# Kernel optimization log

Measured on AMD Instinct MI355X. Metric: run time of the kernel, lower is better.

The kernel has to match this reference:

```python
import jax, jax.numpy as jnp
import numpy as np

COMMITMENT_COST = 0.25
NUM_EMBEDDINGS = 1024
EMBEDDING_DIM = 256


def setup_inputs() -> dict:
    key = jax.random.key(0)
    k1, k2 = jax.random.split(key)
    inputs = jax.random.normal(k1, (64, 256, 32, 32), dtype=jnp.float32)
    emb_w = jax.random.normal(k2, (NUM_EMBEDDINGS, EMBEDDING_DIM), dtype=jnp.float32)
    return {"inputs": inputs, "emb_w": emb_w}


def reference(inputs, emb_w):
    # NCHW -> NHWC, flatten to [N, D]
    x = jnp.transpose(inputs, (0, 2, 3, 1))  # [B, H, W, D]
    B, H, W, D = x.shape
    flat = x.reshape(-1, D)  # [N, D]

    distances = (
        jnp.sum(flat * flat, axis=1, keepdims=True)
        + jnp.sum(emb_w * emb_w, axis=1)
        - 2.0 * flat @ emb_w.T
    )
    idx = jnp.argmin(distances, axis=1)  # [N]

    # one-hot @ W is just a gather of codebook rows
    quantized = emb_w[idx].reshape(B, H, W, D)

    # avg_probs = mean of one-hot encodings = normalized codeword counts
    counts = jnp.zeros((NUM_EMBEDDINGS,), dtype=jnp.float32).at[idx].add(1.0)
    avg_probs = counts / flat.shape[0]
    perplexity = jnp.exp(-jnp.sum(avg_probs * jnp.log(avg_probs + 1e-10)))

    e_latent_loss = jnp.mean((jax.lax.stop_gradient(quantized) - x) ** 2)
    loss = COMMITMENT_COST * e_latent_loss

    # straight-through estimator
    quantized_st = x + jax.lax.stop_gradient(quantized - x)
    quantized_out = jnp.transpose(quantized_st, (0, 3, 1, 2))  # back to NCHW

    return loss, quantized_out, perplexity, idx.reshape(B, H, W)
```

## Files before the change

### kernel.cpp

```cpp
#include <hip/hip_runtime.h>
#include <hip/hip_bf16.h>
#include <math.h>

typedef _Float16 f16;
typedef __attribute__((ext_vector_type(8))) _Float16 f16x8;
typedef __attribute__((ext_vector_type(16))) float f32x16;

#define DIMS 256
#define NCODE 1024
#define NPTS 65536

#define OUT_Q_OFF 1
#define OUT_PERP_OFF 16777217
#define OUT_IDX_OFF 16777218

#define EHI_F32_OFF 4
#define ELO_F32_OFF (4 + 131072)
#define TILE_BYTES 16384

#define XSTRIDE 132

__device__ __forceinline__ void gload_lds16(const void* g, void* l) {
    __builtin_amdgcn_global_load_lds(
        (const __attribute__((address_space(1))) unsigned int*)g,
        (__attribute__((address_space(3))) unsigned int*)l, 16, 0, 0);
}

__global__ __launch_bounds__(256) void k_eprep(const float* __restrict__ ew,
                                               char* __restrict__ ehi,
                                               char* __restrict__ elo,
                                               float* __restrict__ enorm) {
    int w = threadIdx.x >> 6;
    int l = threadIdx.x & 63;
    int row = blockIdx.x * 4 + w;
    float4 v = *reinterpret_cast<const float4*>(ew + (size_t)row * DIMS + l * 4);
    float vv[4] = {v.x, v.y, v.z, v.w};
    __align__(8) f16 hh[4];
    __align__(8) f16 ll[4];
    float s = 0.0f;
    #pragma unroll
    for (int e = 0; e < 4; ++e) {
        f16 h = (f16)vv[e];
        hh[e] = h;
        ll[e] = (f16)(vv[e] - (float)h);
        s += vv[e] * vv[e];
    }
    size_t off = (size_t)(row >> 5) * TILE_BYTES + (size_t)(row & 31) * 512
               + (size_t)((((l >> 1) ^ (row & 7)) << 4) + ((l & 1) << 3));
    *reinterpret_cast<float2*>(ehi + off) = *reinterpret_cast<float2*>(hh);
    *reinterpret_cast<float2*>(elo + off) = *reinterpret_cast<float2*>(ll);
    #pragma unroll
    for (int off2 = 32; off2 > 0; off2 >>= 1) s += __shfl_down(s, off2);
    if (l == 0) enorm[row] = s;
}

__global__ __launch_bounds__(256, 2) void k_argmin_mfma(const float* __restrict__ x,
                                                        const char* __restrict__ ehi,
                                                        const char* __restrict__ elo,
                                                        const float* __restrict__ enorm,
                                                        int* __restrict__ out_idx) {
    __shared__ __align__(16) char smem[2 * 2 * TILE_BYTES];
    __shared__ float enorm_lds[NCODE];
    float* Xs = (float*)smem;

    const int t = threadIdx.x;
    const int wave = t >> 6;
    const int lane = t & 63;
    const int lrow = lane & 31;
    const int lhalf = lane >> 5;

    const int blk = blockIdx.x;
    const int b = blk >> 3;
    const int hw0 = (blk & 7) << 7;
    const float* xb = x + (size_t)b * (DIMS * 1024) + hw0;

    #pragma unroll
    for (int i = 0; i < 4; ++i) enorm_lds[t + 256 * i] = enorm[t + 256 * i];

    f16x8 ahi[16], alo[16];
    #pragma unroll
    for (int dc = 0; dc < 4; ++dc) {
        __syncthreads();
        #pragma unroll
        for (int i = 0; i < 8; ++i) {
            int d = (t >> 5) + 8 * i;
            int p4 = (t & 31) * 4;
            float4 v = *reinterpret_cast<const float4*>(xb + (size_t)(dc * 64 + d) * 1024 + p4);
            *reinterpret_cast<float4*>(&Xs[d * XSTRIDE + p4]) = v;
        }
        __syncthreads();
        int p = wave * 32 + lrow;
        #pragma unroll
        for (int kcl = 0; kcl < 4; ++kcl) {
            f16x8 h, l;
            #pragma unroll
            for (int e = 0; e < 8; ++e) {
                float xv = Xs[(kcl * 16 + lhalf * 8 + e) * XSTRIDE + p];
                f16 hi = (f16)xv;
                h[e] = hi;
                l[e] = (f16)(xv - (float)hi);
            }
            ahi[dc * 4 + kcl] = h;
            alo[dc * 4 + kcl] = l;
        }
    }
    __syncthreads();

    const char* gplane = (wave >> 1) ? elo : ehi;
    const int pl_off = (wave >> 1) * TILE_BYTES;
    const int woff = (wave & 1) * 8192;

    #pragma unroll
    for (int i = 0; i < 8; ++i) {
        int off = woff + i * 1024;
        gload_lds16(gplane + off + lane * 16, smem + pl_off + off);
    }
    __syncthreads();

    float bestv[16];
    int besti[16];
    #pragma unroll
    for (int r = 0; r < 16; ++r) { bestv[r] = 3.4e38f; besti[r] = 0; }

#define ROUND_BODY(ACC_CUR, ACC_PREV, RD)                                         \
    {                                                                             \
        const int rd_ = (RD);                                                     \
        const int cur_ = rd_ & 1;                                                 \
        if (rd_ + 1 < 32) {                                                       \
            const char* gp_ = gplane + (size_t)(rd_ + 1) * TILE_BYTES;            \
            char* lp_ = smem + (cur_ ^ 1) * (2 * TILE_BYTES) + pl_off;            \
            _Pragma("unroll")                                                     \
            for (int i_ = 0; i_ < 8; ++i_) {                                      \
                int off_ = woff + i_ * 1024;                                      \
                gload_lds16(gp_ + off_ + lane * 16, lp_ + off_);                  \
            }                                                                     \
        }                                                                         \
        const char* EHb_ = smem + cur_ * (2 * TILE_BYTES);                        \
        const char* ELb_ = EHb_ + TILE_BYTES;                                     \
        _Pragma("unroll")                                                         \
        for (int r_ = 0; r_ < 16; ++r_) ACC_CUR[r_] = 0.0f;                       \
        __builtin_amdgcn_s_setprio(1);                                            \
        _Pragma("unroll")                                                         \
        for (int kc_ = 0; kc_ < 16; ++kc_) {                                      \
            int g_ = kc_ * 2 + lhalf;                                             \
            int ra_ = lrow * 512 + ((g_ ^ (lrow & 7)) << 4);                      \
            f16x8 bh_ = *reinterpret_cast<const f16x8*>(EHb_ + ra_);              \
            f16x8 bl_ = *reinterpret_cast<const f16x8*>(ELb_ + ra_);              \
            ACC_CUR = __builtin_amdgcn_mfma_f32_32x32x16_f16(ahi[kc_], bh_, ACC_CUR, 0, 0, 0); \
            ACC_CUR = __builtin_amdgcn_mfma_f32_32x32x16_f16(ahi[kc_], bl_, ACC_CUR, 0, 0, 0); \
            ACC_CUR = __builtin_amdgcn_mfma_f32_32x32x16_f16(alo[kc_], bh_, ACC_CUR, 0, 0, 0); \
        }                                                                         \
        __builtin_amdgcn_s_setprio(0);                                            \
        if (rd_ > 0) {                                                            \
            const int pc0_ = (rd_ - 1) * 32;                                      \
            float en_ = enorm_lds[pc0_ + lrow];                                   \
            int cw_ = pc0_ + lrow;                                                \
            _Pragma("unroll")                                                     \
            for (int r_ = 0; r_ < 16; ++r_) {                                     \
                float s_ = fmaf(-2.0f, ACC_PREV[r_], en_);                        \
                if (s_ < bestv[r_]) { bestv[r_] = s_; besti[r_] = cw_; }          \
            }                                                                     \
        }                                                                         \
        __syncthreads();                                                          \
    }

    f32x16 accA, accB;
    for (int rr = 0; rr < 16; ++rr) {
        ROUND_BODY(accA, accB, 2 * rr);
        ROUND_BODY(accB, accA, 2 * rr + 1);
    }
    {
        float en = enorm_lds[31 * 32 + lrow];
        int cw = 31 * 32 + lrow;
        #pragma unroll
        for (int r = 0; r < 16; ++r) {
            float s = fmaf(-2.0f, accB[r], en);
            if (s < bestv[r]) { bestv[r] = s; besti[r] = cw; }
        }
    }
#undef ROUND_BODY

    #pragma unroll
    for (int off = 1; off <= 16; off <<= 1) {
        #pragma unroll
        for (int r = 0; r < 16; ++r) {
            float ov = __shfl_xor(bestv[r], off);
            int oi = __shfl_xor(besti[r], off);
            if (ov < bestv[r] || (ov == bestv[r] && oi < besti[r])) {
                bestv[r] = ov;
                besti[r] = oi;
            }
        }
    }
    if (lrow == 0) {
        #pragma unroll
        for (int r = 0; r < 16; ++r) {
            int row = (r & 3) + 8 * (r >> 2) + 4 * lhalf;
            out_idx[blk * 128 + wave * 32 + row] = besti[r];
        }
    }
}

#define QSTRIDE 258
__global__ __launch_bounds__(512) void k_quant(const float* __restrict__ x,
                                               const float* __restrict__ ew,
                                               const int* __restrict__ idxv,
                                               float* __restrict__ out,
                                               float* __restrict__ loss_acc,
                                               int* __restrict__ counts) {
    __shared__ float Eq[64 * QSTRIDE];
    __shared__ int ids[64];
    __shared__ int h[NCODE];
    const int t = threadIdx.x;
    const int blk = blockIdx.x;
    const int b = blk >> 4;
    const int hw0 = (blk & 15) << 6;

    if (t < 64) ids[t] = idxv[(b << 10) + hw0 + t];
    h[t] = 0;
    h[t + 512] = 0;
    __syncthreads();

    if (t < 64) atomicAdd(&h[ids[t]], 1);

    #pragma unroll
    for (int i = 0; i < 8; ++i) {
        int f = i * 512 + t;
        int row = f >> 6;
        int c4 = f & 63;
        float4 v = *reinterpret_cast<const float4*>(ew + (size_t)ids[row] * DIMS + c4 * 4);
        float2 lo2 = {v.x, v.y};
        float2 hi2 = {v.z, v.w};
        *reinterpret_cast<float2*>(&Eq[row * QSTRIDE + c4 * 4]) = lo2;
        *reinterpret_cast<float2*>(&Eq[row * QSTRIDE + c4 * 4 + 2]) = hi2;
    }
    __syncthreads();

    const int q4 = t & 15;
    const int cb = t >> 4;
    const int p = q4 * 4;
    float lsum = 0.0f;
    #pragma unroll
    for (int k = 0; k < 8; ++k) {
        int c = k * 32 + cb;
        unsigned g = ((unsigned)b << 18) | ((unsigned)c << 10) | (unsigned)(hw0 + p);
        float4 xv = *reinterpret_cast<const float4*>(x + g);
        float q0 = Eq[(p + 0) * QSTRIDE + c];
        float q1 = Eq[(p + 1) * QSTRIDE + c];
        float q2 = Eq[(p + 2) * QSTRIDE + c];
        float q3 = Eq[(p + 3) * QSTRIDE + c];
        float d0 = q0 - xv.x, d1 = q1 - xv.y, d2 = q2 - xv.z, d3 = q3 - xv.w;
        out[OUT_Q_OFF + g + 0] = xv.x + d0;
        out[OUT_Q_OFF + g + 1] = xv.y + d1;
        out[OUT_Q_OFF + g + 2] = xv.z + d2;
        out[OUT_Q_OFF + g + 3] = xv.w + d3;
        lsum += d0 * d0 + d1 * d1 + d2 * d2 + d3 * d3;
    }
    #pragma unroll
    for (int off = 32; off > 0; off >>= 1) lsum += __shfl_down(lsum, off);
    if ((t & 63) == 0) atomicAdd(&loss_acc[blk & 63], lsum);

    int v0 = h[t];
    if (v0) atomicAdd(&counts[t], v0);
    int v1 = h[t + 512];
    if (v1) atomicAdd(&counts[t + 512], v1);
    if (t < 64) out[OUT_IDX_OFF + (b << 10) + hw0 + t] = (float)ids[t];
}

__global__ __launch_bounds__(256) void k_final(const int* __restrict__ counts,
                                               const float* __restrict__ loss_acc,
                                               float* __restrict__ out) {
    int t = threadIdx.x;
    float s = 0.0f;
    #pragma unroll
    for (int i = 0; i < 4; ++i) {
        int cnt = counts[t + 256 * i];
        float p = (float)cnt * (1.0f / 65536.0f);
        s += p * logf(p + 1e-10f);
    }
    #pragma unroll
    for (int off = 32; off > 0; off >>= 1) s += __shfl_down(s, off);
    __shared__ float wsum[4];
    if ((t & 63) == 0) wsum[t >> 6] = s;
    __syncthreads();
    if (t == 0) {
        float S = wsum[0] + wsum[1] + wsum[2] + wsum[3];
        out[OUT_PERP_OFF] = expf(-S);
        float ls = 0.0f;
        for (int i = 0; i < 64; ++i) ls += loss_acc[i];
        out[0] = 0.25f * (ls * (1.0f / 16777216.0f));
    }
}

extern "C" void kernel_launch(void* const* d_in, const int* in_sizes, int n_in,
                              void* d_out, int out_size, void* d_ws, size_t ws_size,
                              hipStream_t stream) {
    const float* x = (const float*)d_in[0];
    const float* ew = (const float*)d_in[1];
    float* out = (float*)d_out;
    float* ws = (float*)d_ws;

    float* loss_acc = ws;
    int* counts = (int*)(ws + 64);
    float* enorm = ws + 64 + 1024;
    int* idxv = (int*)(ws + 64 + 2048);

    char* ehi = (char*)(out + EHI_F32_OFF);
    char* elo = (char*)(out + ELO_F32_OFF);

    hipMemsetAsync(d_ws, 0, (64 + 1024) * sizeof(float), stream);

    k_eprep<<<256, 256, 0, stream>>>(ew, ehi, elo, enorm);
    k_argmin_mfma<<<512, 256, 0, stream>>>(x, ehi, elo, enorm, idxv);
    k_quant<<<1024, 512, 0, stream>>>(x, ew, idxv, out, loss_acc, counts);
    k_final<<<1, 256, 0, stream>>>(counts, loss_acc, out);
}
```

Measured before the change: 173.4 us.

## Fold codebook norm into MFMA init, fuse final reduction, rework quant access

The argmin kernel now seeds each accumulator with -0.5*||e||^2 and tracks a maximum, so the per-element fma in the compare loop goes away. The separate single-block finalize kernel is removed. Its perplexity and loss reduction now run in the last-arriving k_quant block, detected with a global atomic counter, which saves one kernel launch. k_quant also changes from float4 loads of x to scalar coalesced per-channel accesses, and pads the LDS stride to 257 to avoid bank conflicts, at the cost of narrower global transactions.

New measurement: 389.7 us. +124.8%, slower.

```diff
diff --git a/kernel.cpp b/kernel.cpp
--- a/kernel.cpp
+++ b/kernel.cpp
@@ -120,7 +120,7 @@
     float bestv[16];
     int besti[16];
     #pragma unroll
-    for (int r = 0; r < 16; ++r) { bestv[r] = 3.4e38f; besti[r] = 0; }
+    for (int r = 0; r < 16; ++r) { bestv[r] = -3.4e38f; besti[r] = 0; }
 
 #define ROUND_BODY(ACC_CUR, ACC_PREV, RD)                                         \
     {                                                                             \
@@ -137,8 +137,9 @@
         }                                                                         \
         const char* EHb_ = smem + cur_ * (2 * TILE_BYTES);                        \
         const char* ELb_ = EHb_ + TILE_BYTES;                                     \
+        float nh_ = -0.5f * enorm_lds[rd_ * 32 + lrow];                           \
         _Pragma("unroll")                                                         \
-        for (int r_ = 0; r_ < 16; ++r_) ACC_CUR[r_] = 0.0f;                       \
+        for (int r_ = 0; r_ < 16; ++r_) ACC_CUR[r_] = nh_;                        \
         __builtin_amdgcn_s_setprio(1);                                            \
         _Pragma("unroll")                                                         \
         for (int kc_ = 0; kc_ < 16; ++kc_) {                                      \
@@ -152,13 +153,11 @@
         }                                                                         \
         __builtin_amdgcn_s_setprio(0);                                            \
         if (rd_ > 0) {                                                            \
-            const int pc0_ = (rd_ - 1) * 32;                                      \
-            float en_ = enorm_lds[pc0_ + lrow];                                   \
-            int cw_ = pc0_ + lrow;                                                \
+            const int cw_ = (rd_ - 1) * 32 + lrow;                                \
             _Pragma("unroll")                                                     \
             for (int r_ = 0; r_ < 16; ++r_) {                                     \
-                float s_ = fmaf(-2.0f, ACC_PREV[r_], en_);                        \
-                if (s_ < bestv[r_]) { bestv[r_] = s_; besti[r_] = cw_; }          \
+                float s_ = ACC_PREV[r_];                                          \
+                if (s_ > bestv[r_]) { bestv[r_] = s_; besti[r_] = cw_; }          \
             }                                                                     \
         }                                                                         \
         __syncthreads();                                                          \
@@ -170,12 +169,11 @@
         ROUND_BODY(accB, accA, 2 * rr + 1);
     }
     {
-        float en = enorm_lds[31 * 32 + lrow];
         int cw = 31 * 32 + lrow;
         #pragma unroll
         for (int r = 0; r < 16; ++r) {
-            float s = fmaf(-2.0f, accB[r], en);
-            if (s < bestv[r]) { bestv[r] = s; besti[r] = cw; }
+            float s = accB[r];
+            if (s > bestv[r]) { bestv[r] = s; besti[r] = cw; }
         }
     }
 #undef ROUND_BODY
@@ -186,7 +184,7 @@
         for (int r = 0; r < 16; ++r) {
             float ov = __shfl_xor(bestv[r], off);
             int oi = __shfl_xor(besti[r], off);
-            if (ov < bestv[r] || (ov == bestv[r] && oi < besti[r])) {
+            if (ov > bestv[r] || (ov == bestv[r] && oi < besti[r])) {
                 bestv[r] = ov;
                 besti[r] = oi;
             }
@@ -201,16 +199,18 @@
     }
 }
 
-#define QSTRIDE 258
+#define QSTRIDE 257
 __global__ __launch_bounds__(512) void k_quant(const float* __restrict__ x,
                                                const float* __restrict__ ew,
                                                const int* __restrict__ idxv,
                                                float* __restrict__ out,
                                                float* __restrict__ loss_acc,
-                                               int* __restrict__ counts) {
+                                               int* __restrict__ counts,
+                                               int* __restrict__ ctr) {
     __shared__ float Eq[64 * QSTRIDE];
     __shared__ int ids[64];
     __shared__ int h[NCODE];
+    __shared__ int amlast;
     const int t = threadIdx.x;
     const int blk = blockIdx.x;
     const int b = blk >> 4;
@@ -218,7 +218,7 @@
 
     if (t < 64) ids[t] = idxv[(b << 10) + hw0 + t];
     h[t] = 0;
-    h[t + 512] = 0;
+    if (t < NCODE - 512) h[t + 512] = 0;
     __syncthreads();
 
     if (t < 64) atomicAdd(&h[ids[t]], 1);
@@ -229,62 +229,58 @@
         int row = f >> 6;
         int c4 = f & 63;
         float4 v = *reinterpret_cast<const float4*>(ew + (size_t)ids[row] * DIMS + c4 * 4);
-        float2 lo2 = {v.x, v.y};
-        float2 hi2 = {v.z, v.w};
-        *reinterpret_cast<float2*>(&Eq[row * QSTRIDE + c4 * 4]) = lo2;
-        *reinterpret_cast<float2*>(&Eq[row * QSTRIDE + c4 * 4 + 2]) = hi2;
-    }
-    __syncthreads();
-
-    const int q4 = t & 15;
-    const int cb = t >> 4;
-    const int p = q4 * 4;
+        Eq[row * QSTRIDE + c4 * 4 + 0] = v.x;
+        Eq[row * QSTRIDE + c4 * 4 + 1] = v.y;
+        Eq[row * QSTRIDE + c4 * 4 + 2] = v.z;
+        Eq[row * QSTRIDE + c4 * 4 + 3] = v.w;
+    }
+    __syncthreads();
+
+    const int wave = t >> 6;
+    const int p = t & 63;
     float lsum = 0.0f;
     #pragma unroll
-    for (int k = 0; k < 8; ++k) {
-        int c = k * 32 + cb;
+    for (int k = 0; k < 32; ++k) {
+        int c = wave * 32 + k;
         unsigned g = ((unsigned)b << 18) | ((unsigned)c << 10) | (unsigned)(hw0 + p);
-        float4 xv = *reinterpret_cast<const float4*>(x + g);
-        float q0 = Eq[(p + 0) * QSTRIDE + c];
-        float q1 = Eq[(p + 1) * QSTRIDE + c];
-        float q2 = Eq[(p + 2) * QSTRIDE + c];
-        float q3 = Eq[(p + 3) * QSTRIDE + c];
-        float d0 = q0 - xv.x, d1 = q1 - xv.y, d2 = q2 - xv.z, d3 = q3 - xv.w;
-        out[OUT_Q_OFF + g + 0] = xv.x + d0;
-        out[OUT_Q_OFF + g + 1] = xv.y + d1;
-        out[OUT_Q_OFF + g + 2] = xv.z + d2;
-        out[OUT_Q_OFF + g + 3] = xv.w + d3;
-        lsum += d0 * d0 + d1 * d1 + d2 * d2 + d3 * d3;
+        float xv = x[g];
+        float q = Eq[p * QSTRIDE + c];
+        float d = q - xv;
+        out[OUT_Q_OFF + g] = xv + d;
+        lsum += d * d;
     }
     #pragma unroll
     for (int off = 32; off > 0; off >>= 1) lsum += __shfl_down(lsum, off);
-    if ((t & 63) == 0) atomicAdd(&loss_acc[blk & 63], lsum);
+    if (p == 0) atomicAdd(&loss_acc[blk & 63], lsum);
 
     int v0 = h[t];
     if (v0) atomicAdd(&counts[t], v0);
-    int v1 = h[t + 512];
-    if (v1) atomicAdd(&counts[t + 512], v1);
+    if (t < NCODE - 512) {
+        int v1 = h[t + 512];
+        if (v1) atomicAdd(&counts[t + 512], v1);
+    }
     if (t < 64) out[OUT_IDX_OFF + (b << 10) + hw0 + t] = (float)ids[t];
-}
-
-__global__ __launch_bounds__(256) void k_final(const int* __restrict__ counts,
-                                               const float* __restrict__ loss_acc,
-                                               float* __restrict__ out) {
-    int t = threadIdx.x;
+
+    __threadfence();
+    if (t == 0) amlast = (atomicAdd(ctr, 1) == 1023);
+    __syncthreads();
+    if (!amlast) return;
+
     float s = 0.0f;
     #pragma unroll
-    for (int i = 0; i < 4; ++i) {
-        int cnt = counts[t + 256 * i];
-        float p = (float)cnt * (1.0f / 65536.0f);
-        s += p * logf(p + 1e-10f);
+    for (int i = 0; i < 2; ++i) {
+        int cnt = counts[t + 512 * i];
+        float pp = (float)cnt * (1.0f / 65536.0f);
+        s += pp * logf(pp + 1e-10f);
     }
     #pragma unroll
     for (int off = 32; off > 0; off >>= 1) s += __shfl_down(s, off);
-    __shared__ float wsum[4];
+    __shared__ float wsum[8];
     if ((t & 63) == 0) wsum[t >> 6] = s;
     __syncthreads();
     if (t == 0) {
-        float S = wsum[0] + wsum[1] + wsum[2] + wsum[3];
+        float S = 0.0f;
+        for (int i = 0; i < 8; ++i) S += wsum[i];
         out[OUT_PERP_OFF] = expf(-S);
         float ls = 0.0f;
         for (int i = 0; i < 64; ++i) ls += loss_acc[i];
@@ -302,16 +298,16 @@
 
     float* loss_acc = ws;
     int* counts = (int*)(ws + 64);
-    float* enorm = ws + 64 + 1024;
-    int* idxv = (int*)(ws + 64 + 2048);
+    int* ctr = (int*)(ws + 64 + 1024);
+    float* enorm = ws + 64 + 1024 + 4;
+    int* idxv = (int*)(ws + 64 + 1024 + 4 + 1024);
 
     char* ehi = (char*)(out + EHI_F32_OFF);
     char* elo = (char*)(out + ELO_F32_OFF);
 
-    hipMemsetAsync(d_ws, 0, (64 + 1024) * sizeof(float), stream);
+    hipMemsetAsync(d_ws, 0, (64 + 1024 + 4) * sizeof(float), stream);
 
     k_eprep<<<256, 256, 0, stream>>>(ew, ehi, elo, enorm);
     k_argmin_mfma<<<512, 256, 0, stream>>>(x, ehi, elo, enorm, idxv);
-    k_quant<<<1024, 512, 0, stream>>>(x, ew, idxv, out, loss_acc, counts);
-    k_final<<<1, 256, 0, stream>>>(counts, loss_acc, out);
-}
+    k_quant<<<1024, 512, 0, stream>>>(x, ew, idxv, out, loss_acc, counts, ctr);
+}
```
